# Optimization experiments

Hardware: AMD Instinct MI355X
Metric: run time of the kernel (lower is better)

Reference implementation:

```python
import jax, jax.numpy as jnp
import numpy as np

D = 192      # model dim (out_channels)
DIN = 384    # d_inner = 2*D
N = 16       # d_state
DTR = 12     # dt_rank = ceil(D/16)
K = 4        # depthwise conv kernel size
NB = 3       # total mamba blocks (2 stacked + 1 in downsample)


def setup_inputs() -> dict:
    key = jax.random.key(0)
    ks = jax.random.split(key, 8)
    rn = lambda k, shape, s: jax.random.normal(k, shape, jnp.float32) * s
    inp = {
        "x": jax.random.normal(ks[0], (2, 96, 56, 56), jnp.float32),
        "proj_w": rn(ks[1], (D, 96), 0.1),
        "proj_b": jnp.zeros((D,), jnp.float32),
        "bn_g": jnp.ones((D,), jnp.float32),
        "bn_b": jnp.zeros((D,), jnp.float32),
        "bn_mean": jnp.zeros((D,), jnp.float32),
        "bn_var": jnp.ones((D,), jnp.float32),
        "ln_g": jnp.ones((NB, D), jnp.float32),
        "ln_b": jnp.zeros((NB, D), jnp.float32),
        "Win": rn(ks[2], (NB, 2 * DIN, D), 0.05),
        "b_in": jnp.zeros((NB, 2 * DIN), jnp.float32),
        "conv_w": rn(ks[3], (NB, DIN, K), 0.2),
        "conv_b": jnp.zeros((NB, DIN), jnp.float32),
        "Wx": rn(ks[4], (NB, DTR + 2 * N, DIN), 0.05),
        "Wdt": rn(ks[5], (NB, DIN, DTR), 0.05),
        "bdt": jnp.full((NB, DIN), -4.6, jnp.float32),  # softplus ~ 0.01
        "A_log": jnp.log(jnp.broadcast_to(jnp.arange(1, N + 1, dtype=jnp.float32), (NB, DIN, N))),
        "Dskip": jnp.ones((NB, DIN), jnp.float32),
        "Wout": rn(ks[6], (NB, D, DIN), 0.05),
        "bout": jnp.zeros((NB, D), jnp.float32),
    }
    return inp


def _mamba(x, ln_g, ln_b, Win, b_in, conv_w, conv_b, Wx, Wdt, bdt, A_log, Dskip, Wout, bout):
    # x: (B, C, H, W) -> flatten spatial dims to a sequence (B, L, C)
    B, C, H, W = x.shape
    L = H * W
    seq = x.reshape(B, C, L).transpose(0, 2, 1)
    mu = seq.mean(-1, keepdims=True)
    var = seq.var(-1, keepdims=True)
    h = (seq - mu) * jax.lax.rsqrt(var + 1e-5) * ln_g + ln_b  # LayerNorm
    xz = jnp.einsum('bld,ed->ble', h, Win) + b_in              # (B, L, 2*DIN)
    xi, z = jnp.split(xz, 2, axis=-1)
    # depthwise causal conv1d along L
    xc = jnp.pad(xi.transpose(0, 2, 1), ((0, 0), (0, 0), (K - 1, 0)))
    xc = jax.lax.conv_general_dilated(xc, conv_w[:, None, :], (1,), 'VALID',
                                      feature_group_count=DIN) + conv_b[:, None]
    xi = jax.nn.silu(xc).transpose(0, 2, 1)                    # (B, L, DIN)
    proj = jnp.einsum('ble,pe->blp', xi, Wx)                   # (B, L, DTR+2N)
    dtl = proj[..., :DTR]
    Bm = proj[..., DTR:DTR + N]
    Cm = proj[..., DTR + N:]
    dt = jax.nn.softplus(jnp.einsum('blr,er->ble', dtl, Wdt) + bdt)  # (B, L, DIN)
    A = -jnp.exp(A_log)                                         # (DIN, N)
    dA = jnp.exp(dt[..., None] * A)                             # (B, L, DIN, N)
    dBx = (dt * xi)[..., None] * Bm[:, :, None, :]              # (B, L, DIN, N)

    def step(hc, t):
        dA_t, dBx_t, C_t = t
        hc = dA_t * hc + dBx_t                                  # (B, DIN, N)
        return hc, jnp.einsum('ben,bn->be', hc, C_t)

    h0 = jnp.zeros((B, DIN, N), x.dtype)
    _, ys = jax.lax.scan(step, h0, (dA.transpose(1, 0, 2, 3),
                                    dBx.transpose(1, 0, 2, 3),
                                    Cm.transpose(1, 0, 2)))
    y = ys.transpose(1, 0, 2) + Dskip * xi
    y = y * jax.nn.silu(z)
    out = jnp.einsum('ble,de->bld', y, Wout) + bout
    return out.transpose(0, 2, 1).reshape(B, C, H, W)


def _maxpool2(x):
    return jax.lax.reduce_window(x, -jnp.inf, jax.lax.max,
                                 (1, 1, 2, 2), (1, 1, 2, 2), 'VALID')


def reference(x, proj_w, proj_b, bn_g, bn_b, bn_mean, bn_var, ln_g, ln_b, Win, b_in,
              conv_w, conv_b, Wx, Wdt, bdt, A_log, Dskip, Wout, bout):
    # proj (conv1x1) + BatchNorm (eval-mode running stats)
    x = jnp.einsum('bchw,oc->bohw', x, proj_w) + proj_b[:, None, None]
    x = (x - bn_mean[:, None, None]) * jax.lax.rsqrt(bn_var[:, None, None] + 1e-5) \
        * bn_g[:, None, None] + bn_b[:, None, None]
    blk = lambda i, v: _mamba(v, ln_g[i], ln_b[i], Win[i], b_in[i], conv_w[i], conv_b[i],
                              Wx[i], Wdt[i], bdt[i], A_log[i], Dskip[i], Wout[i], bout[i])
    for i in range(2):  # residual mamba blocks
        x = x + blk(i, x)
    skip = x
    x = blk(2, _maxpool2(x))  # downsample: maxpool then mamba (no residual)
    return (x, skip)
```

## Files before the change

kernel.cpp:

```cpp
#include <hip/hip_runtime.h>

typedef __attribute__((ext_vector_type(8))) __bf16 bf16x8;
typedef __attribute__((ext_vector_type(4))) __bf16 bf16x4;
typedef __attribute__((ext_vector_type(4))) float f32x4;

#define DEV static __device__ __forceinline__

DEV float fast_rcp(float x) { return __builtin_amdgcn_rcpf(x); }
DEV float sigm(float x) { return fast_rcp(1.f + __expf(-x)); }
DEV float siluf(float x) { return x * sigm(x); }
DEV float softplusf(float x) { return x > 20.f ? x : __logf(1.f + __expf(x)); }

__global__ __launch_bounds__(256) void k_proj_wcvt(
    const float* __restrict__ x, const float* __restrict__ pw,
    const float* __restrict__ pb, const float* __restrict__ bng,
    const float* __restrict__ bnb, const float* __restrict__ bnm,
    const float* __restrict__ bnv, float* __restrict__ v,
    const float* __restrict__ Win, const float* __restrict__ Wout,
    const float* __restrict__ Wx, __bf16* __restrict__ Wb)
{
  constexpr int SAP = 104;
  __shared__ __bf16 As[64 * SAP];
  __shared__ __bf16 Ws[64 * SAP];
  const int tid = threadIdx.x;
  const int bid = blockIdx.x;

  if (bid >= 294) {
    const int idx = (bid - 294) * 256 + tid;
    if (idx < 442368) Wb[idx] = (__bf16)Win[idx];
    else if (idx < 663552) Wb[idx] = (__bf16)Wout[idx - 442368];
    else Wb[idx] = (__bf16)Wx[idx - 663552];
    return;
  }

  const int r0 = (bid % 98) * 64;
  const int col0 = (bid / 98) * 64;
  const int b = r0 / 3136, l0 = r0 % 3136;
  const int lane = tid & 63, wv = tid >> 6;
  const int rh = wv >> 1, ch = wv & 1;
  const int lm = lane & 15, quad = lane >> 4;

#pragma unroll
  for (int it = 0; it < 6; ++it) {
    const int idx = tid + it * 256;
    const int c = idx >> 4, l4 = idx & 15;
    const float4 t = *(const float4*)(x + ((size_t)(b * 96 + c)) * 3136 + l0 + l4 * 4);
    As[(l4 * 4 + 0) * SAP + c] = (__bf16)t.x;
    As[(l4 * 4 + 1) * SAP + c] = (__bf16)t.y;
    As[(l4 * 4 + 2) * SAP + c] = (__bf16)t.z;
    As[(l4 * 4 + 3) * SAP + c] = (__bf16)t.w;
  }
#pragma unroll
  for (int it = 0; it < 6; ++it) {
    const int idx = tid + it * 256;
    const int wr = idx / 24, kc = (idx % 24) * 4;
    const float4 t = *(const float4*)(pw + (size_t)(col0 + wr) * 96 + kc);
    bf16x4 o;
    o[0] = (__bf16)t.x; o[1] = (__bf16)t.y; o[2] = (__bf16)t.z; o[3] = (__bf16)t.w;
    *(bf16x4*)(&Ws[wr * SAP + kc]) = o;
  }
  __syncthreads();

  f32x4 acc[2][2] = {};
#pragma unroll
  for (int ks = 0; ks < 3; ++ks) {
    const int kb = ks * 32 + quad * 8;
    bf16x8 a0 = *(const bf16x8*)(&As[(rh * 32 + lm) * SAP + kb]);
    bf16x8 a1 = *(const bf16x8*)(&As[(rh * 32 + 16 + lm) * SAP + kb]);
    bf16x8 b0 = *(const bf16x8*)(&Ws[(ch * 32 + lm) * SAP + kb]);
    bf16x8 b1 = *(const bf16x8*)(&Ws[(ch * 32 + 16 + lm) * SAP + kb]);
    acc[0][0] = __builtin_amdgcn_mfma_f32_16x16x32_bf16(a0, b0, acc[0][0], 0, 0, 0);
    acc[0][1] = __builtin_amdgcn_mfma_f32_16x16x32_bf16(a0, b1, acc[0][1], 0, 0, 0);
    acc[1][0] = __builtin_amdgcn_mfma_f32_16x16x32_bf16(a1, b0, acc[1][0], 0, 0, 0);
    acc[1][1] = __builtin_amdgcn_mfma_f32_16x16x32_bf16(a1, b1, acc[1][1], 0, 0, 0);
  }

#pragma unroll
  for (int ti = 0; ti < 2; ++ti)
#pragma unroll
    for (int tj = 0; tj < 2; ++tj) {
      const int gcol = col0 + ch * 32 + tj * 16 + lm;
      const float s = rsqrtf(bnv[gcol] + 1e-5f) * bng[gcol];
      const float sh = (pb[gcol] - bnm[gcol]) * s + bnb[gcol];
#pragma unroll
      for (int j = 0; j < 4; ++j) {
        const int grow = r0 + rh * 32 + ti * 16 + quad * 4 + j;
        v[(size_t)grow * 192 + gcol] = acc[ti][tj][j] * s + sh;
      }
    }
}

__global__ __launch_bounds__(256) void k_conv(
    const float* __restrict__ xz, __bf16* __restrict__ xiB,
    const float* __restrict__ cw, const float* __restrict__ cb,
    int Lseq, int nthreads)
{
  const int idx = blockIdx.x * 256 + threadIdx.x;
  if (idx >= nthreads) return;
  const int e = idx % 384;
  const int seg = idx / 384;
  const int nseg = Lseq / 8;
  const int b = seg / nseg;
  const int l0 = (seg % nseg) * 8;
  const float4 w4 = *(const float4*)(cw + e * 4);
  const float bv = cb[e];
  float xv[11];
#pragma unroll
  for (int k = 0; k < 11; ++k) {
    const int l = l0 - 3 + k;
    xv[k] = (l >= 0) ? xz[(size_t)(b * Lseq + l) * 768 + e] : 0.f;
  }
#pragma unroll
  for (int j = 0; j < 8; ++j) {
    const float a = bv + xv[j] * w4.x + xv[j + 1] * w4.y + xv[j + 2] * w4.z + xv[j + 3] * w4.w;
    xiB[(size_t)(b * Lseq + l0 + j) * 384 + e] = (__bf16)siluf(a);
  }
}

constexpr int EPI_XZ = 0, EPI_G2 = 1, EPI_RES = 2, EPI_RES_SKIP = 3, EPI_OUT2 = 4;

template <int AMODE, int NT, int EPI>
__global__ __launch_bounds__(256) void k_gemm(
    const void* __restrict__ Ain, const __bf16* __restrict__ W,
    const float* __restrict__ bias, float* __restrict__ O,
    int M, int K, int Nvalid,
    float* __restrict__ dtlbuf, float* __restrict__ bcbuf,
    float* __restrict__ oflt,
    const float* __restrict__ lng, const float* __restrict__ lnb,
    int Lseq)
{
  constexpr int SA = 200;
  constexpr int CT = (NT == 1) ? 2 : 4;
  __shared__ __bf16 As[64 * SA];
  __shared__ __bf16 Ws[64 * NT * SA];
  __shared__ float lnS[(AMODE >= 2) ? 384 : 1];
  const int tid = threadIdx.x;
  const int r0 = blockIdx.x * 64;
  const int col0 = blockIdx.y * (64 * NT);
  const int lane = tid & 63, wv = tid >> 6;
  const int rh = (NT == 1) ? (wv >> 1) : (wv & 1);
  const int ch = (NT == 1) ? (wv & 1) : (wv >> 1);
  const int lm = lane & 15, quad = lane >> 4;

  if constexpr (AMODE >= 2) {
    if (tid < 192) { lnS[tid] = lng[tid]; lnS[192 + tid] = lnb[tid]; }
    __syncthreads();
  }

  f32x4 acc[2][CT] = {};
  const int nkp = K / 192;
  for (int kp = 0; kp < nkp; ++kp) {
    if (kp) __syncthreads();
    if constexpr (AMODE == 1) {
      const __bf16* Ab = (const __bf16*)Ain;
#pragma unroll
      for (int it = 0; it < 6; ++it) {
        const int idx = tid + it * 256;
        const int row = idx / 24, kc = (idx % 24) * 8;
        const int gr = min(r0 + row, M - 1);
        bf16x8 val = *(const bf16x8*)(Ab + (size_t)gr * K + kp * 192 + kc);
        *(bf16x8*)(&As[row * SA + kc]) = val;
      }
    } else {
      const float* A = (const float*)Ain;
      const int row = tid >> 2, part = tid & 3;
      const int gr = min(r0 + row, M - 1);
      const int cbase = part * 48;
      float4 tv[12];
      if constexpr (AMODE == 2) {
#pragma unroll
        for (int j = 0; j < 12; ++j)
          tv[j] = *(const float4*)(A + (size_t)gr * 192 + cbase + j * 4);
      } else {
        const int bb = gr / 784, l2 = gr % 784;
        const int h2 = l2 / 28, w2 = l2 % 28;
        const float* p0 = A + (size_t)(bb * 3136 + h2 * 112 + w2 * 2) * 192;
#pragma unroll
        for (int j = 0; j < 12; ++j) {
          const int cc = cbase + j * 4;
          const float4 a0 = *(const float4*)(p0 + cc);
          const float4 a1 = *(const float4*)(p0 + 192 + cc);
          const float4 a2 = *(const float4*)(p0 + 56 * 192 + cc);
          const float4 a3 = *(const float4*)(p0 + 57 * 192 + cc);
          tv[j].x = fmaxf(fmaxf(a0.x, a1.x), fmaxf(a2.x, a3.x));
          tv[j].y = fmaxf(fmaxf(a0.y, a1.y), fmaxf(a2.y, a3.y));
          tv[j].z = fmaxf(fmaxf(a0.z, a1.z), fmaxf(a2.z, a3.z));
          tv[j].w = fmaxf(fmaxf(a0.w, a1.w), fmaxf(a2.w, a3.w));
        }
      }
      float s = 0.f, sq = 0.f;
#pragma unroll
      for (int j = 0; j < 12; ++j) {
        s += tv[j].x + tv[j].y + tv[j].z + tv[j].w;
        sq += tv[j].x * tv[j].x + tv[j].y * tv[j].y + tv[j].z * tv[j].z + tv[j].w * tv[j].w;
      }
      s += __shfl_xor(s, 1); s += __shfl_xor(s, 2);
      sq += __shfl_xor(sq, 1); sq += __shfl_xor(sq, 2);
      const float mean = s * (1.f / 192.f);
      const float rstd = rsqrtf(sq * (1.f / 192.f) - mean * mean + 1e-5f);
#pragma unroll
      for (int j = 0; j < 12; ++j) {
        const int c = cbase + j * 4;
        bf16x4 o;
        o[0] = (__bf16)((tv[j].x - mean) * rstd * lnS[c + 0] + lnS[192 + c + 0]);
        o[1] = (__bf16)((tv[j].y - mean) * rstd * lnS[c + 1] + lnS[192 + c + 1]);
        o[2] = (__bf16)((tv[j].z - mean) * rstd * lnS[c + 2] + lnS[192 + c + 2]);
        o[3] = (__bf16)((tv[j].w - mean) * rstd * lnS[c + 3] + lnS[192 + c + 3]);
        *(bf16x4*)(&As[row * SA + c]) = o;
      }
    }
#pragma unroll
    for (int it = 0; it < 6 * NT; ++it) {
      const int idx = tid + it * 256;
      const int wr = idx / 24, kc = (idx % 24) * 8;
      const int gw = col0 + wr;
      bf16x8 val = {};
      if (gw < Nvalid) val = *(const bf16x8*)(W + (size_t)gw * K + kp * 192 + kc);
      *(bf16x8*)(&Ws[wr * SA + kc]) = val;
    }
    __syncthreads();
#pragma unroll
    for (int ks = 0; ks < 6; ++ks) {
      const int kb = ks * 32 + quad * 8;
      bf16x8 a0 = *(const bf16x8*)(&As[(rh * 32 + lm) * SA + kb]);
      bf16x8 a1 = *(const bf16x8*)(&As[(rh * 32 + 16 + lm) * SA + kb]);
#pragma unroll
      for (int tj = 0; tj < CT; ++tj) {
        bf16x8 bfr = *(const bf16x8*)(&Ws[(ch * (16 * CT) + tj * 16 + lm) * SA + kb]);
        acc[0][tj] = __builtin_amdgcn_mfma_f32_16x16x32_bf16(a0, bfr, acc[0][tj], 0, 0, 0);
        acc[1][tj] = __builtin_amdgcn_mfma_f32_16x16x32_bf16(a1, bfr, acc[1][tj], 0, 0, 0);
      }
    }
  }

  if constexpr (EPI == EPI_G2) {
    __shared__ float dtlS[64 * 12];
#pragma unroll
    for (int ti = 0; ti < 2; ++ti)
#pragma unroll
      for (int tj = 0; tj < CT; ++tj) {
        const int colt = ch * (16 * CT) + tj * 16 + lm;
#pragma unroll
        for (int j = 0; j < 4; ++j) {
          const int rowt = rh * 32 + ti * 16 + quad * 4 + j;
          const int grow = r0 + rowt;
          const float val = acc[ti][tj][j];
          if (colt < 12) dtlS[rowt * 12 + colt] = val;
          else if (colt < 44 && grow < M)
            bcbuf[(size_t)grow * 32 + (colt - 12)] = val;
        }
      }
    __syncthreads();
    for (int idx = tid; idx < 64 * 12; idx += 256) {
      const int grow = r0 + idx / 12;
      if (grow < M) dtlbuf[(size_t)grow * 12 + idx % 12] = dtlS[idx];
    }
  } else {
#pragma unroll
    for (int ti = 0; ti < 2; ++ti)
#pragma unroll
      for (int tj = 0; tj < CT; ++tj) {
        const int colt = ch * (16 * CT) + tj * 16 + lm;
        const int gcol = col0 + colt;
        const float bv = bias[gcol];
#pragma unroll
        for (int j = 0; j < 4; ++j) {
          const int rowt = rh * 32 + ti * 16 + quad * 4 + j;
          const int grow = r0 + rowt;
          if (grow >= M) continue;
          const float val = acc[ti][tj][j] + bv;
          if constexpr (EPI == EPI_XZ) {
            O[(size_t)grow * 768 + gcol] = val;
          } else if constexpr (EPI == EPI_RES) {
            O[(size_t)grow * 192 + gcol] += val;
          } else if constexpr (EPI == EPI_RES_SKIP) {
            const float nv = O[(size_t)grow * 192 + gcol] + val;
            O[(size_t)grow * 192 + gcol] = nv;
            const int b = grow / 3136, l = grow % 3136;
            oflt[b * 602112 + gcol * 3136 + l] = nv;
          } else {
            const int b = grow / 784, l = grow % 784;
            oflt[b * 150528 + gcol * 784 + l] = val;
          }
        }
      }
  }
}

constexpr int SC_LC = 14, SC_T = 7, SC_TN = 2;

DEV void compute_dts(const float* __restrict__ dtl, const float* __restrict__ Wdt,
                     const float* __restrict__ bdt, int rowbase, int e, int t,
                     float* dtlS, float* wdtS)
{
  for (int idx = t; idx < SC_LC * 12; idx += 128)
    dtlS[idx] = dtl[(size_t)(rowbase + idx / 12) * 12 + idx % 12];
#pragma unroll
  for (int r = 0; r < 12; ++r) wdtS[r * 128 + t] = Wdt[(size_t)e * 12 + r];
}

__global__ __launch_bounds__(128) void k_scan1(
    const float* __restrict__ dtl, const __bf16* __restrict__ xi,
    const float* __restrict__ bc, const float* __restrict__ Wdt,
    const float* __restrict__ bdt, const float* __restrict__ A_log,
    float* __restrict__ DT, float* __restrict__ S, int Lseq, int NC)
{
  __shared__ float Bs[SC_LC * 16];
  __shared__ float dts[SC_LC * 128];
  __shared__ float dtlS[SC_LC * 12];
  __shared__ float wdtS[12 * 128];
  const int t = threadIdx.x;
  const int e = blockIdx.y * 128 + t;
  const int c = blockIdx.x % NC;
  const int b = blockIdx.x / NC;
  const int rowbase = b * Lseq + c * SC_LC;

  for (int idx = t; idx < SC_LC * 16; idx += 128) {
    const int l = idx >> 4, q = idx & 15;
    Bs[idx] = bc[(size_t)(rowbase + l) * 32 + q];
  }
  compute_dts(dtl, Wdt, bdt, rowbase, e, t, dtlS, wdtS);
  const float bdte = bdt[e];

  float An2[16];
  {
    const float4* a4 = (const float4*)(A_log + e * 16);
    float4 t0 = a4[0], t1 = a4[1], t2 = a4[2], t3 = a4[3];
    float tmp[16] = {t0.x, t0.y, t0.z, t0.w, t1.x, t1.y, t1.z, t1.w,
                     t2.x, t2.y, t2.z, t2.w, t3.x, t3.y, t3.z, t3.w};
#pragma unroll
    for (int n = 0; n < 16; ++n) An2[n] = -__expf(tmp[n]) * 1.44269504f;
  }
  __syncthreads();
  float dtsum = 0.f;
  for (int l = 0; l < SC_LC; ++l) {
    float a = bdte;
#pragma unroll
    for (int r = 0; r < 12; ++r) a += dtlS[l * 12 + r] * wdtS[r * 128 + t];
    const float sp = softplusf(a);
    dts[l * 128 + t] = sp;
    dtsum += sp;
  }

  float h[16];
#pragma unroll
  for (int n = 0; n < 16; ++n) h[n] = 0.f;

  float xA[SC_T], xB[SC_T];
  auto LOADA = [&](int tt) {
#pragma unroll
    for (int j = 0; j < SC_T; ++j)
      xA[j] = (float)xi[(size_t)(rowbase + tt * SC_T + j) * 384 + e];
  };
  auto LOADB = [&](int tt) {
#pragma unroll
    for (int j = 0; j < SC_T; ++j)
      xB[j] = (float)xi[(size_t)(rowbase + tt * SC_T + j) * 384 + e];
  };
  auto COMP = [&](const float (&x8)[SC_T], int tt) {
#pragma unroll
    for (int j = 0; j < SC_T; ++j) {
      const int l = tt * SC_T + j;
      const float dtv = dts[l * 128 + t];
      const float u = dtv * x8[j];
      const float* Brow = &Bs[l * 16];
#pragma unroll
      for (int n = 0; n < 16; ++n) {
        const float a = __builtin_amdgcn_exp2f(dtv * An2[n]);
        h[n] = a * h[n] + u * Brow[n];
      }
    }
  };

  LOADA(0);
#pragma unroll
  for (int tt = 0; tt < SC_TN; ++tt) {
    if (tt & 1) { if (tt + 1 < SC_TN) LOADA(tt + 1); COMP(xB, tt); }
    else        { if (tt + 1 < SC_TN) LOADB(tt + 1); COMP(xA, tt); }
  }

  const size_t o = ((size_t)(b * NC + c) * 384 + e) * 16;
#pragma unroll
  for (int q = 0; q < 4; ++q)
    *(float4*)(S + o + q * 4) = make_float4(h[q*4], h[q*4+1], h[q*4+2], h[q*4+3]);
  DT[(size_t)(b * NC + c) * 384 + e] = dtsum;
}

__global__ __launch_bounds__(256) void k_carry(
    const float* __restrict__ DT, float* __restrict__ SH,
    const float* __restrict__ A_log, int NC)
{
  const int tid = blockIdx.x * 256 + threadIdx.x;
  const int b = tid / 6144, r = tid % 6144;
  const float An2 = -__expf(A_log[r]) * 1.44269504f;
  const size_t o = (size_t)b * NC * 6144 + r;
  const size_t od = (size_t)b * NC * 384 + (r >> 4);

  float sA[8], dA[8], sB[8], dB[8];
  auto LOAD = [&](float (&sv)[8], float (&dv)[8], int c0) {
#pragma unroll
    for (int k = 0; k < 8; ++k) {
      sv[k] = SH[o + (size_t)(c0 + k) * 6144];
      dv[k] = DT[od + (size_t)(c0 + k) * 384];
    }
  };
  float h = 0.f;
  auto COMP = [&](const float (&sv)[8], const float (&dv)[8], int c0) {
    float a[8];
#pragma unroll
    for (int k = 0; k < 8; ++k) a[k] = __builtin_amdgcn_exp2f(An2 * dv[k]);
#pragma unroll
    for (int k = 0; k < 8; ++k) {
      SH[o + (size_t)(c0 + k) * 6144] = h;
      h = a[k] * h + sv[k];
    }
  };

  LOAD(sA, dA, 0);
  for (int c0 = 0; c0 < NC; c0 += 16) {
    if (c0 + 8 < NC) LOAD(sB, dB, c0 + 8);
    COMP(sA, dA, c0);
    if (c0 + 8 < NC) {
      if (c0 + 16 < NC) LOAD(sA, dA, c0 + 16);
      COMP(sB, dB, c0 + 8);
    }
  }
}

__global__ __launch_bounds__(128) void k_scan2(
    const float* __restrict__ dtl, const __bf16* __restrict__ xi,
    const float* __restrict__ bc, const float* __restrict__ xz,
    const float* __restrict__ Wdt, const float* __restrict__ bdt,
    const float* __restrict__ A_log, const float* __restrict__ Dskip,
    const float* __restrict__ H0, __bf16* __restrict__ y, int Lseq, int NC)
{
  __shared__ float BCs[SC_LC * 32];
  __shared__ float dts[SC_LC * 128];
  __shared__ float dtlS[SC_LC * 12];
  __shared__ float wdtS[12 * 128];
  const int t = threadIdx.x;
  const int e = blockIdx.y * 128 + t;
  const int c = blockIdx.x % NC;
  const int b = blockIdx.x / NC;
  const int rowbase = b * Lseq + c * SC_LC;

  for (int idx = t; idx < SC_LC * 32; idx += 128)
    BCs[idx] = bc[(size_t)rowbase * 32 + idx];
  compute_dts(dtl, Wdt, bdt, rowbase, e, t, dtlS, wdtS);
  const float bdte = bdt[e];

  float An2[16];
  {
    const float4* a4 = (const float4*)(A_log + e * 16);
    float4 t0 = a4[0], t1 = a4[1], t2 = a4[2], t3 = a4[3];
    float tmp[16] = {t0.x, t0.y, t0.z, t0.w, t1.x, t1.y, t1.z, t1.w,
                     t2.x, t2.y, t2.z, t2.w, t3.x, t3.y, t3.z, t3.w};
#pragma unroll
    for (int n = 0; n < 16; ++n) An2[n] = -__expf(tmp[n]) * 1.44269504f;
  }
  float h[16];
  {
    const size_t o = ((size_t)(b * NC + c) * 384 + e) * 16;
    const float4* h4 = (const float4*)(H0 + o);
    float4 t0 = h4[0], t1 = h4[1], t2 = h4[2], t3 = h4[3];
    h[0]=t0.x; h[1]=t0.y; h[2]=t0.z; h[3]=t0.w;
    h[4]=t1.x; h[5]=t1.y; h[6]=t1.z; h[7]=t1.w;
    h[8]=t2.x; h[9]=t2.y; h[10]=t2.z; h[11]=t2.w;
    h[12]=t3.x; h[13]=t3.y; h[14]=t3.z; h[15]=t3.w;
  }
  __syncthreads();
  for (int l = 0; l < SC_LC; ++l) {
    float a = bdte;
#pragma unroll
    for (int r = 0; r < 12; ++r) a += dtlS[l * 12 + r] * wdtS[r * 128 + t];
    dts[l * 128 + t] = softplusf(a);
  }
  const float Dse = Dskip[e];

  float xA[SC_T], zA[SC_T], xB[SC_T], zB[SC_T];
  auto LOADA = [&](int tt) {
#pragma unroll
    for (int j = 0; j < SC_T; ++j) {
      const size_t r = (size_t)(rowbase + tt * SC_T + j);
      xA[j] = (float)xi[r * 384 + e];
      zA[j] = xz[r * 768 + 384 + e];
    }
  };
  auto LOADB = [&](int tt) {
#pragma unroll
    for (int j = 0; j < SC_T; ++j) {
      const size_t r = (size_t)(rowbase + tt * SC_T + j);
      xB[j] = (float)xi[r * 384 + e];
      zB[j] = xz[r * 768 + 384 + e];
    }
  };
  auto COMP = [&](const float (&x8)[SC_T], const float (&z8)[SC_T], int tt) {
#pragma unroll
    for (int j = 0; j < SC_T; ++j) {
      const int l = tt * SC_T + j;
      const float dtv = dts[l * 128 + t];
      const float xiv = x8[j];
      const float u = dtv * xiv;
      const float* Brow = &BCs[l * 32];
      const float* Crow = Brow + 16;
      float yv = 0.f;
#pragma unroll
      for (int n = 0; n < 16; ++n) {
        const float a = __builtin_amdgcn_exp2f(dtv * An2[n]);
        h[n] = a * h[n] + u * Brow[n];
        yv += h[n] * Crow[n];
      }
      y[(size_t)(rowbase + l) * 384 + e] = (__bf16)((yv + Dse * xiv) * siluf(z8[j]));
    }
  };

  LOADA(0);
#pragma unroll
  for (int tt = 0; tt < SC_TN; ++tt) {
    if (tt & 1) { if (tt + 1 < SC_TN) LOADA(tt + 1); COMP(xB, zB, tt); }
    else        { if (tt + 1 < SC_TN) LOADB(tt + 1); COMP(xA, zA, tt); }
  }
}

extern "C" void kernel_launch(void* const* d_in, const int* in_sizes, int n_in,
                              void* d_out, int out_size, void* d_ws, size_t ws_size,
                              hipStream_t stream)
{
  const float* x    = (const float*)d_in[0];
  const float* pw   = (const float*)d_in[1];
  const float* pb   = (const float*)d_in[2];
  const float* bng  = (const float*)d_in[3];
  const float* bnb  = (const float*)d_in[4];
  const float* bnm  = (const float*)d_in[5];
  const float* bnv  = (const float*)d_in[6];
  const float* lng  = (const float*)d_in[7];
  const float* lnb  = (const float*)d_in[8];
  const float* Win  = (const float*)d_in[9];
  const float* b_in = (const float*)d_in[10];
  const float* cw   = (const float*)d_in[11];
  const float* cb   = (const float*)d_in[12];
  const float* Wx   = (const float*)d_in[13];
  const float* Wdt  = (const float*)d_in[14];
  const float* bdt  = (const float*)d_in[15];
  const float* Alog = (const float*)d_in[16];
  const float* Dsk  = (const float*)d_in[17];
  const float* Wout = (const float*)d_in[18];
  const float* bout = (const float*)d_in[19];

  float* wsf = (float*)d_ws;
  float* v    = wsf;
  float* xz   = v + 1204224;
  float* dtlb = xz + 4816896;
  float* bcb  = dtlb + 75264;
  float* Sb   = bcb + 200704;
  float* Pb   = Sb + 2752512;
  __bf16* xiB = (__bf16*)(Pb + 2752512);
  __bf16* yB  = (__bf16*)(Pb + 2752512 + 1204224);
  __bf16* Wb  = (__bf16*)(Pb + 2752512 + 2408448);

  float* out0 = (float*)d_out;
  float* out1 = out0 + 301056;

  k_proj_wcvt<<<3084, 256, 0, stream>>>(x, pw, pb, bng, bnb, bnm, bnv, v,
                                        Win, Wout, Wx, Wb);

  for (int i = 0; i < 3; ++i) {
    const int big = (i < 2) ? 1 : 0;
    const int Lseq = big ? 3136 : 784;
    const int M = 2 * Lseq;
    const int NC = Lseq / SC_LC;
    const int MB = (M + 63) / 64;
    const float* lng_i = lng + i * 192;
    const float* lnb_i = lnb + i * 192;
    const float* bin_i = b_in + i * 768;
    const float* cw_i  = cw + i * 384 * 4;
    const float* cb_i  = cb + i * 384;
    const float* Wdt_i = Wdt + i * 384 * 12;
    const float* bdt_i = bdt + i * 384;
    const float* Al_i  = Alog + i * 384 * 16;
    const float* Ds_i  = Dsk + i * 384;
    const float* bo_i  = bout + i * 192;
    const __bf16* Winb_i  = Wb + i * 147456;
    const __bf16* Woutb_i = Wb + 442368 + i * 73728;
    const __bf16* Wxb_i   = Wb + 663552 + i * 16896;

    if (big)
      k_gemm<2, 2, EPI_XZ><<<dim3(MB, 6), 256, 0, stream>>>(
          v, Winb_i, bin_i, xz, M, 192, 768,
          nullptr, nullptr, nullptr, lng_i, lnb_i, Lseq);
    else
      k_gemm<3, 2, EPI_XZ><<<dim3(MB, 6), 256, 0, stream>>>(
          v, Winb_i, bin_i, xz, M, 192, 768,
          nullptr, nullptr, nullptr, lng_i, lnb_i, Lseq);
    k_conv<<<(M * 384 / 8 + 255) / 256, 256, 0, stream>>>(
        xz, xiB, cw_i, cb_i, Lseq, M * 384 / 8);
    k_gemm<1, 1, EPI_G2><<<dim3(MB, 1), 256, 0, stream>>>(
        xiB, Wxb_i, nullptr, nullptr, M, 384, 44,
        dtlb, bcb, nullptr, nullptr, nullptr, Lseq);
    k_scan1<<<dim3(2 * NC, 3), 128, 0, stream>>>(
        dtlb, xiB, bcb, Wdt_i, bdt_i, Al_i, Pb, Sb, Lseq, NC);
    k_carry<<<48, 256, 0, stream>>>(Pb, Sb, Al_i, NC);
    k_scan2<<<dim3(2 * NC, 3), 128, 0, stream>>>(
        dtlb, xiB, bcb, xz, Wdt_i, bdt_i, Al_i, Ds_i, Sb, yB, Lseq, NC);
    if (i == 0)
      k_gemm<1, 1, EPI_RES><<<dim3(MB, 3), 256, 0, stream>>>(
          yB, Woutb_i, bo_i, v, M, 384, 192,
          nullptr, nullptr, nullptr, nullptr, nullptr, Lseq);
    else if (i == 1)
      k_gemm<1, 1, EPI_RES_SKIP><<<dim3(MB, 3), 256, 0, stream>>>(
          yB, Woutb_i, bo_i, v, M, 384, 192,
          nullptr, nullptr, out1, nullptr, nullptr, Lseq);
    else
      k_gemm<1, 1, EPI_OUT2><<<dim3(MB, 3), 256, 0, stream>>>(
          yB, Woutb_i, bo_i, v, M, 384, 192,
          nullptr, nullptr, out0, nullptr, nullptr, Lseq);
  }
}
```

Before: 358.4 us.

## Fuse depthwise causal conv and SiLU into in-projection GEMM epilogue

```diff
diff --git a/kernel.cpp b/kernel.cpp
--- a/kernel.cpp
+++ b/kernel.cpp
@@ -10,6 +10,7 @@
 DEV float sigm(float x) { return fast_rcp(1.f + __expf(-x)); }
 DEV float siluf(float x) { return x * sigm(x); }
 DEV float softplusf(float x) { return x > 20.f ? x : __logf(1.f + __expf(x)); }
+
 
 __global__ __launch_bounds__(256) void k_proj_wcvt(
     const float* __restrict__ x, const float* __restrict__ pw,
@@ -26,10 +27,18 @@
   const int bid = blockIdx.x;
 
   if (bid >= 294) {
-    const int idx = (bid - 294) * 256 + tid;
-    if (idx < 442368) Wb[idx] = (__bf16)Win[idx];
-    else if (idx < 663552) Wb[idx] = (__bf16)Wout[idx - 442368];
-    else Wb[idx] = (__bf16)Wx[idx - 663552];
+    const int idx = ((bid - 294) * 256 + tid) * 4;
+    if (idx < 714240) {
+      const float* src;
+      if (idx < 442368) src = Win + idx;
+      else if (idx < 663552) src = Wout + (idx - 442368);
+      else src = Wx + (idx - 663552);
+      const float4 tv = *(const float4*)src;
+      bf16x4 o;
+      o[0] = (__bf16)tv.x; o[1] = (__bf16)tv.y;
+      o[2] = (__bf16)tv.z; o[3] = (__bf16)tv.w;
+      *(bf16x4*)(Wb + idx) = o;
+    }
     return;
   }
 
@@ -90,33 +99,6 @@
     }
 }
 
-__global__ __launch_bounds__(256) void k_conv(
-    const float* __restrict__ xz, __bf16* __restrict__ xiB,
-    const float* __restrict__ cw, const float* __restrict__ cb,
-    int Lseq, int nthreads)
-{
-  const int idx = blockIdx.x * 256 + threadIdx.x;
-  if (idx >= nthreads) return;
-  const int e = idx % 384;
-  const int seg = idx / 384;
-  const int nseg = Lseq / 8;
-  const int b = seg / nseg;
-  const int l0 = (seg % nseg) * 8;
-  const float4 w4 = *(const float4*)(cw + e * 4);
-  const float bv = cb[e];
-  float xv[11];
-#pragma unroll
-  for (int k = 0; k < 11; ++k) {
-    const int l = l0 - 3 + k;
-    xv[k] = (l >= 0) ? xz[(size_t)(b * Lseq + l) * 768 + e] : 0.f;
-  }
-#pragma unroll
-  for (int j = 0; j < 8; ++j) {
-    const float a = bv + xv[j] * w4.x + xv[j + 1] * w4.y + xv[j + 2] * w4.z + xv[j + 3] * w4.w;
-    xiB[(size_t)(b * Lseq + l0 + j) * 384 + e] = (__bf16)siluf(a);
-  }
-}
-
 constexpr int EPI_XZ = 0, EPI_G2 = 1, EPI_RES = 2, EPI_RES_SKIP = 3, EPI_OUT2 = 4;
 
 template <int AMODE, int NT, int EPI>
@@ -127,13 +109,22 @@
     float* __restrict__ dtlbuf, float* __restrict__ bcbuf,
     float* __restrict__ oflt,
     const float* __restrict__ lng, const float* __restrict__ lnb,
-    int Lseq)
+    int Lseq, const float* __restrict__ cw, const float* __restrict__ cbv)
 {
   constexpr int SA = 200;
   constexpr int CT = (NT == 1) ? 2 : 4;
-  __shared__ __bf16 As[64 * SA];
-  __shared__ __bf16 Ws[64 * NT * SA];
-  __shared__ float lnS[(AMODE >= 2) ? 384 : 1];
+  constexpr int A_ROWS = (AMODE >= 2) ? 67 : 64;
+  constexpr int ABYTES = A_ROWS * SA * 2;
+  constexpr int WBYTES = 64 * NT * SA * 2;
+  constexpr int LBYTES = (AMODE >= 2) ? 384 * 4 : 0;
+  constexpr int XBYTES = (EPI == EPI_XZ) ? 67 * 132 * 4 : (EPI == EPI_G2 ? 64 * 12 * 4 : 0);
+  constexpr int MAINB = ABYTES + WBYTES + LBYTES;
+  constexpr int SMEMB = MAINB > XBYTES ? MAINB : XBYTES;
+  __shared__ __align__(16) char smem[SMEMB];
+  __bf16* As = (__bf16*)smem;
+  __bf16* Ws = (__bf16*)(smem + ABYTES);
+  float* lnS = (float*)(smem + ABYTES + WBYTES);
+
   const int tid = threadIdx.x;
   const int r0 = blockIdx.x * 64;
   const int col0 = blockIdx.y * (64 * NT);
@@ -163,50 +154,60 @@
       }
     } else {
       const float* A = (const float*)Ain;
-      const int row = tid >> 2, part = tid & 3;
-      const int gr = min(r0 + row, M - 1);
+      const int part = tid & 3;
       const int cbase = part * 48;
-      float4 tv[12];
-      if constexpr (AMODE == 2) {
-#pragma unroll
-        for (int j = 0; j < 12; ++j)
-          tv[j] = *(const float4*)(A + (size_t)gr * 192 + cbase + j * 4);
-      } else {
-        const int bb = gr / 784, l2 = gr % 784;
-        const int h2 = l2 / 28, w2 = l2 % 28;
-        const float* p0 = A + (size_t)(bb * 3136 + h2 * 112 + w2 * 2) * 192;
+      auto STAGE_ROW = [&](int row_slot, int gr) {
+        float4 tv[12];
+        if constexpr (AMODE == 2) {
+#pragma unroll
+          for (int j = 0; j < 12; ++j)
+            tv[j] = *(const float4*)(A + (size_t)gr * 192 + cbase + j * 4);
+        } else {
+          const int bb = gr / 784, l2 = gr % 784;
+          const int h2 = l2 / 28, w2 = l2 % 28;
+          const float* p0 = A + (size_t)(bb * 3136 + h2 * 112 + w2 * 2) * 192;
+#pragma unroll
+          for (int j = 0; j < 12; ++j) {
+            const int cc2 = cbase + j * 4;
+            const float4 a0 = *(const float4*)(p0 + cc2);
+            const float4 a1 = *(const float4*)(p0 + 192 + cc2);
+            const float4 a2 = *(const float4*)(p0 + 56 * 192 + cc2);
+            const float4 a3 = *(const float4*)(p0 + 57 * 192 + cc2);
+            tv[j].x = fmaxf(fmaxf(a0.x, a1.x), fmaxf(a2.x, a3.x));
+            tv[j].y = fmaxf(fmaxf(a0.y, a1.y), fmaxf(a2.y, a3.y));
+            tv[j].z = fmaxf(fmaxf(a0.z, a1.z), fmaxf(a2.z, a3.z));
+            tv[j].w = fmaxf(fmaxf(a0.w, a1.w), fmaxf(a2.w, a3.w));
+          }
+        }
+        float s = 0.f, sq = 0.f;
 #pragma unroll
         for (int j = 0; j < 12; ++j) {
-          const int cc = cbase + j * 4;
-          const float4 a0 = *(const float4*)(p0 + cc);
-          const float4 a1 = *(const float4*)(p0 + 192 + cc);
-          const float4 a2 = *(const float4*)(p0 + 56 * 192 + cc);
-          const float4 a3 = *(const float4*)(p0 + 57 * 192 + cc);
-          tv[j].x = fmaxf(fmaxf(a0.x, a1.x), fmaxf(a2.x, a3.x));
-          tv[j].y = fmaxf(fmaxf(a0.y, a1.y), fmaxf(a2.y, a3.y));
-          tv[j].z = fmaxf(fmaxf(a0.z, a1.z), fmaxf(a2.z, a3.z));
-          tv[j].w = fmaxf(fmaxf(a0.w, a1.w), fmaxf(a2.w, a3.w));
-        }
-      }
-      float s = 0.f, sq = 0.f;
-#pragma unroll
-      for (int j = 0; j < 12; ++j) {
-        s += tv[j].x + tv[j].y + tv[j].z + tv[j].w;
-        sq += tv[j].x * tv[j].x + tv[j].y * tv[j].y + tv[j].z * tv[j].z + tv[j].w * tv[j].w;
-      }
-      s += __shfl_xor(s, 1); s += __shfl_xor(s, 2);
-      sq += __shfl_xor(sq, 1); sq += __shfl_xor(sq, 2);
-      const float mean = s * (1.f / 192.f);
-      const float rstd = rsqrtf(sq * (1.f / 192.f) - mean * mean + 1e-5f);
-#pragma unroll
-      for (int j = 0; j < 12; ++j) {
-        const int c = cbase + j * 4;
-        bf16x4 o;
-        o[0] = (__bf16)((tv[j].x - mean) * rstd * lnS[c + 0] + lnS[192 + c + 0]);
-        o[1] = (__bf16)((tv[j].y - mean) * rstd * lnS[c + 1] + lnS[192 + c + 1]);
-        o[2] = (__bf16)((tv[j].z - mean) * rstd * lnS[c + 2] + lnS[192 + c + 2]);
-        o[3] = (__bf16)((tv[j].w - mean) * rstd * lnS[c + 3] + lnS[192 + c + 3]);
-        *(bf16x4*)(&As[row * SA + c]) = o;
+          s += tv[j].x + tv[j].y + tv[j].z + tv[j].w;
+          sq += tv[j].x * tv[j].x + tv[j].y * tv[j].y + tv[j].z * tv[j].z + tv[j].w * tv[j].w;
+        }
+        s += __shfl_xor(s, 1); s += __shfl_xor(s, 2);
+        sq += __shfl_xor(sq, 1); sq += __shfl_xor(sq, 2);
+        const float mean = s * (1.f / 192.f);
+        const float rstd = rsqrtf(sq * (1.f / 192.f) - mean * mean + 1e-5f);
+#pragma unroll
+        for (int j = 0; j < 12; ++j) {
+          const int c = cbase + j * 4;
+          bf16x4 o;
+          o[0] = (__bf16)((tv[j].x - mean) * rstd * lnS[c + 0] + lnS[192 + c + 0]);
+          o[1] = (__bf16)((tv[j].y - mean) * rstd * lnS[c + 1] + lnS[192 + c + 1]);
+          o[2] = (__bf16)((tv[j].z - mean) * rstd * lnS[c + 2] + lnS[192 + c + 2]);
+          o[3] = (__bf16)((tv[j].w - mean) * rstd * lnS[c + 3] + lnS[192 + c + 3]);
+          *(bf16x4*)(&As[row_slot * SA + c]) = o;
+        }
+      };
+      STAGE_ROW(tid >> 2, min(r0 + (tid >> 2), M - 1));
+      if constexpr (EPI == EPI_XZ) {
+        if (tid < 12) {
+          const int hrow = tid >> 2;
+          int gh = r0 - 3 + hrow;
+          gh = gh < 0 ? 0 : gh;
+          STAGE_ROW(64 + hrow, gh);
+        }
       }
     }
 #pragma unroll
@@ -234,7 +235,8 @@
   }
 
   if constexpr (EPI == EPI_G2) {
-    __shared__ float dtlS[64 * 12];
+    __syncthreads();
+    float* dtlS = (float*)smem;
 #pragma unroll
     for (int ti = 0; ti < 2; ++ti)
 #pragma unroll
@@ -255,6 +257,80 @@
       const int grow = r0 + idx / 12;
       if (grow < M) dtlbuf[(size_t)grow * 12 + idx % 12] = dtlS[idx];
     }
+  } else if constexpr (EPI == EPI_XZ) {
+    if (AMODE >= 2 && col0 < 384) {
+      auto HDOT = [&](int hr, int hc) -> float {
+        const __bf16* ap = &As[(64 + hr) * SA];
+        const __bf16* wp = &Ws[hc * SA];
+        float d = 0.f;
+#pragma unroll
+        for (int k8 = 0; k8 < 24; ++k8) {
+          bf16x8 av = *(const bf16x8*)(ap + k8 * 8);
+          bf16x8 wv8 = *(const bf16x8*)(wp + k8 * 8);
+#pragma unroll
+          for (int u = 0; u < 8; ++u) d += (float)av[u] * (float)wv8[u];
+        }
+        return d + bias[col0 + hc];
+      };
+      const int hr0 = tid >> 7, hc0 = tid & 127;
+      const bool has1 = tid < 128;
+      const float hv0 = HDOT(hr0, hc0);
+      float hv1 = 0.f;
+      if (has1) hv1 = HDOT(2, hc0);
+      __syncthreads();
+      float* xcS = (float*)smem;
+#pragma unroll
+      for (int ti = 0; ti < 2; ++ti)
+#pragma unroll
+        for (int tj = 0; tj < CT; ++tj) {
+          const int colt = ch * (16 * CT) + tj * 16 + lm;
+          const float bv = bias[col0 + colt];
+#pragma unroll
+          for (int j = 0; j < 4; ++j) {
+            const int rowt = rh * 32 + ti * 16 + quad * 4 + j;
+            xcS[(rowt + 3) * 132 + colt] = acc[ti][tj][j] + bv;
+          }
+        }
+      xcS[hr0 * 132 + hc0] = hv0;
+      if (has1) xcS[2 * 132 + hc0] = hv1;
+      __syncthreads();
+      const int cc = tid & 127;
+      const int rbase = tid >> 7;
+      const int gcol = col0 + cc;
+      const float4 w4 = *(const float4*)(cw + gcol * 4);
+      const float cbe = cbv[gcol];
+      __bf16* xout = (__bf16*)oflt;
+#pragma unroll
+      for (int k2 = 0; k2 < 32; ++k2) {
+        const int lt = rbase + k2 * 2;
+        const int grow = r0 + lt;
+        if (grow >= M) break;
+        const int l = grow < Lseq ? grow : grow - Lseq;
+        const float* xp = &xcS[lt * 132 + cc];
+        float a = cbe;
+        a += (l >= 3 ? xp[0]   : 0.f) * w4.x;
+        a += (l >= 2 ? xp[132] : 0.f) * w4.y;
+        a += (l >= 1 ? xp[264] : 0.f) * w4.z;
+        a += xp[396] * w4.w;
+        xout[(size_t)grow * 384 + gcol] = (__bf16)siluf(a);
+      }
+    } else {
+#pragma unroll
+      for (int ti = 0; ti < 2; ++ti)
+#pragma unroll
+        for (int tj = 0; tj < CT; ++tj) {
+          const int colt = ch * (16 * CT) + tj * 16 + lm;
+          const int gcol = col0 + colt;
+          const float bv = bias[gcol];
+#pragma unroll
+          for (int j = 0; j < 4; ++j) {
+            const int rowt = rh * 32 + ti * 16 + quad * 4 + j;
+            const int grow = r0 + rowt;
+            if (grow >= M) continue;
+            O[(size_t)grow * 768 + gcol] = acc[ti][tj][j] + bv;
+          }
+        }
+    }
   } else {
 #pragma unroll
     for (int ti = 0; ti < 2; ++ti)
@@ -269,9 +345,7 @@
           const int grow = r0 + rowt;
           if (grow >= M) continue;
           const float val = acc[ti][tj][j] + bv;
-          if constexpr (EPI == EPI_XZ) {
-            O[(size_t)grow * 768 + gcol] = val;
-          } else if constexpr (EPI == EPI_RES) {
+          if constexpr (EPI == EPI_RES) {
             O[(size_t)grow * 192 + gcol] += val;
           } else if constexpr (EPI == EPI_RES_SKIP) {
             const float nv = O[(size_t)grow * 192 + gcol] + val;
@@ -561,8 +635,8 @@
   float* out0 = (float*)d_out;
   float* out1 = out0 + 301056;
 
-  k_proj_wcvt<<<3084, 256, 0, stream>>>(x, pw, pb, bng, bnb, bnm, bnv, v,
-                                        Win, Wout, Wx, Wb);
+  k_proj_wcvt<<<992, 256, 0, stream>>>(x, pw, pb, bng, bnb, bnm, bnv, v,
+                                       Win, Wout, Wx, Wb);
 
   for (int i = 0; i < 3; ++i) {
     const int big = (i < 2) ? 1 : 0;
@@ -587,16 +661,14 @@
     if (big)
       k_gemm<2, 2, EPI_XZ><<<dim3(MB, 6), 256, 0, stream>>>(
           v, Winb_i, bin_i, xz, M, 192, 768,
-          nullptr, nullptr, nullptr, lng_i, lnb_i, Lseq);
+          nullptr, nullptr, (float*)xiB, lng_i, lnb_i, Lseq, cw_i, cb_i);
     else
       k_gemm<3, 2, EPI_XZ><<<dim3(MB, 6), 256, 0, stream>>>(
           v, Winb_i, bin_i, xz, M, 192, 768,
-          nullptr, nullptr, nullptr, lng_i, lnb_i, Lseq);
-    k_conv<<<(M * 384 / 8 + 255) / 256, 256, 0, stream>>>(
-        xz, xiB, cw_i, cb_i, Lseq, M * 384 / 8);
+          nullptr, nullptr, (float*)xiB, lng_i, lnb_i, Lseq, cw_i, cb_i);
     k_gemm<1, 1, EPI_G2><<<dim3(MB, 1), 256, 0, stream>>>(
         xiB, Wxb_i, nullptr, nullptr, M, 384, 44,
-        dtlb, bcb, nullptr, nullptr, nullptr, Lseq);
+        dtlb, bcb, nullptr, nullptr, nullptr, Lseq, nullptr, nullptr);
     k_scan1<<<dim3(2 * NC, 3), 128, 0, stream>>>(
         dtlb, xiB, bcb, Wdt_i, bdt_i, Al_i, Pb, Sb, Lseq, NC);
     k_carry<<<48, 256, 0, stream>>>(Pb, Sb, Al_i, NC);
@@ -605,14 +677,14 @@
     if (i == 0)
       k_gemm<1, 1, EPI_RES><<<dim3(MB, 3), 256, 0, stream>>>(
           yB, Woutb_i, bo_i, v, M, 384, 192,
-          nullptr, nullptr, nullptr, nullptr, nullptr, Lseq);
+          nullptr, nullptr, nullptr, nullptr, nullptr, Lseq, nullptr, nullptr);
     else if (i == 1)
       k_gemm<1, 1, EPI_RES_SKIP><<<dim3(MB, 3), 256, 0, stream>>>(
           yB, Woutb_i, bo_i, v, M, 384, 192,
-          nullptr, nullptr, out1, nullptr, nullptr, Lseq);
+          nullptr, nullptr, out1, nullptr, nullptr, Lseq, nullptr, nullptr);
     else
       k_gemm<1, 1, EPI_OUT2><<<dim3(MB, 3), 256, 0, stream>>>(
           yB, Woutb_i, bo_i, v, M, 384, 192,
-          nullptr, nullptr, out0, nullptr, nullptr, Lseq);
+          nullptr, nullptr, out0, nullptr, nullptr, Lseq, nullptr, nullptr);
   }
 }
```

New measurement: 392.8 us. 9.6% more time.

## Split xz GEMM into dedicated kernel reading weights directly, vectorize weight conversion

Applied to the files above, without the earlier changes.

```diff
diff --git a/kernel.cpp b/kernel.cpp
--- a/kernel.cpp
+++ b/kernel.cpp
@@ -10,6 +10,7 @@
 DEV float sigm(float x) { return fast_rcp(1.f + __expf(-x)); }
 DEV float siluf(float x) { return x * sigm(x); }
 DEV float softplusf(float x) { return x > 20.f ? x : __logf(1.f + __expf(x)); }
+
 
 __global__ __launch_bounds__(256) void k_proj_wcvt(
     const float* __restrict__ x, const float* __restrict__ pw,
@@ -26,10 +27,18 @@
   const int bid = blockIdx.x;
 
   if (bid >= 294) {
-    const int idx = (bid - 294) * 256 + tid;
-    if (idx < 442368) Wb[idx] = (__bf16)Win[idx];
-    else if (idx < 663552) Wb[idx] = (__bf16)Wout[idx - 442368];
-    else Wb[idx] = (__bf16)Wx[idx - 663552];
+    const int idx = ((bid - 294) * 256 + tid) * 4;
+    if (idx < 714240) {
+      const float* src;
+      if (idx < 442368) src = Win + idx;
+      else if (idx < 663552) src = Wout + (idx - 442368);
+      else src = Wx + (idx - 663552);
+      const float4 tv = *(const float4*)src;
+      bf16x4 o;
+      o[0] = (__bf16)tv.x; o[1] = (__bf16)tv.y;
+      o[2] = (__bf16)tv.z; o[3] = (__bf16)tv.w;
+      *(bf16x4*)(Wb + idx) = o;
+    }
     return;
   }
 
@@ -117,100 +126,138 @@
   }
 }
 
-constexpr int EPI_XZ = 0, EPI_G2 = 1, EPI_RES = 2, EPI_RES_SKIP = 3, EPI_OUT2 = 4;
-
-template <int AMODE, int NT, int EPI>
+template <int AMODE>
+__global__ __launch_bounds__(256, 4) void k_gemm_xz(
+    const float* __restrict__ A, const __bf16* __restrict__ W,
+    const float* __restrict__ bias, float* __restrict__ O,
+    int M, const float* __restrict__ lng, const float* __restrict__ lnb)
+{
+  constexpr int SA = 200;
+  __shared__ __bf16 As[64 * SA];
+  __shared__ float lnS[384];
+  const int tid = threadIdx.x;
+  const int r0 = blockIdx.x * 64;
+  const int col0 = blockIdx.y * 128;
+  const int lane = tid & 63, wv = tid >> 6;
+  const int rh = wv & 1, ch = wv >> 1;
+  const int lm = lane & 15, quad = lane >> 4;
+
+  if (tid < 192) { lnS[tid] = lng[tid]; lnS[192 + tid] = lnb[tid]; }
+  __syncthreads();
+
+  {
+    const int row = tid >> 2, part = tid & 3;
+    const int gr = min(r0 + row, M - 1);
+    const int cbase = part * 48;
+    float4 tv[12];
+    if constexpr (AMODE == 2) {
+#pragma unroll
+      for (int j = 0; j < 12; ++j)
+        tv[j] = *(const float4*)(A + (size_t)gr * 192 + cbase + j * 4);
+    } else {
+      const int bb = gr / 784, l2 = gr % 784;
+      const int h2 = l2 / 28, w2 = l2 % 28;
+      const float* p0 = A + (size_t)(bb * 3136 + h2 * 112 + w2 * 2) * 192;
+#pragma unroll
+      for (int j = 0; j < 12; ++j) {
+        const int cc = cbase + j * 4;
+        const float4 a0 = *(const float4*)(p0 + cc);
+        const float4 a1 = *(const float4*)(p0 + 192 + cc);
+        const float4 a2 = *(const float4*)(p0 + 56 * 192 + cc);
+        const float4 a3 = *(const float4*)(p0 + 57 * 192 + cc);
+        tv[j].x = fmaxf(fmaxf(a0.x, a1.x), fmaxf(a2.x, a3.x));
+        tv[j].y = fmaxf(fmaxf(a0.y, a1.y), fmaxf(a2.y, a3.y));
+        tv[j].z = fmaxf(fmaxf(a0.z, a1.z), fmaxf(a2.z, a3.z));
+        tv[j].w = fmaxf(fmaxf(a0.w, a1.w), fmaxf(a2.w, a3.w));
+      }
+    }
+    float s = 0.f, sq = 0.f;
+#pragma unroll
+    for (int j = 0; j < 12; ++j) {
+      s += tv[j].x + tv[j].y + tv[j].z + tv[j].w;
+      sq += tv[j].x * tv[j].x + tv[j].y * tv[j].y + tv[j].z * tv[j].z + tv[j].w * tv[j].w;
+    }
+    s += __shfl_xor(s, 1); s += __shfl_xor(s, 2);
+    sq += __shfl_xor(sq, 1); sq += __shfl_xor(sq, 2);
+    const float mean = s * (1.f / 192.f);
+    const float rstd = rsqrtf(sq * (1.f / 192.f) - mean * mean + 1e-5f);
+#pragma unroll
+    for (int j = 0; j < 12; ++j) {
+      const int c = cbase + j * 4;
+      bf16x4 o;
+      o[0] = (__bf16)((tv[j].x - mean) * rstd * lnS[c + 0] + lnS[192 + c + 0]);
+      o[1] = (__bf16)((tv[j].y - mean) * rstd * lnS[c + 1] + lnS[192 + c + 1]);
+      o[2] = (__bf16)((tv[j].z - mean) * rstd * lnS[c + 2] + lnS[192 + c + 2]);
+      o[3] = (__bf16)((tv[j].w - mean) * rstd * lnS[c + 3] + lnS[192 + c + 3]);
+      *(bf16x4*)(&As[row * SA + c]) = o;
+    }
+  }
+  __syncthreads();
+
+  f32x4 acc[2][4] = {};
+#pragma unroll
+  for (int ks = 0; ks < 6; ++ks) {
+    const int kb = ks * 32 + quad * 8;
+    bf16x8 a0 = *(const bf16x8*)(&As[(rh * 32 + lm) * SA + kb]);
+    bf16x8 a1 = *(const bf16x8*)(&As[(rh * 32 + 16 + lm) * SA + kb]);
+#pragma unroll
+    for (int tj = 0; tj < 4; ++tj) {
+      const int gw = col0 + ch * 64 + tj * 16 + lm;
+      bf16x8 bfr = *(const bf16x8*)(W + (size_t)gw * 192 + kb);
+      acc[0][tj] = __builtin_amdgcn_mfma_f32_16x16x32_bf16(a0, bfr, acc[0][tj], 0, 0, 0);
+      acc[1][tj] = __builtin_amdgcn_mfma_f32_16x16x32_bf16(a1, bfr, acc[1][tj], 0, 0, 0);
+    }
+  }
+
+#pragma unroll
+  for (int ti = 0; ti < 2; ++ti)
+#pragma unroll
+    for (int tj = 0; tj < 4; ++tj) {
+      const int gcol = col0 + ch * 64 + tj * 16 + lm;
+      const float bv = bias[gcol];
+#pragma unroll
+      for (int j = 0; j < 4; ++j) {
+        const int rowt = rh * 32 + ti * 16 + quad * 4 + j;
+        const int grow = r0 + rowt;
+        if (grow < M) O[(size_t)grow * 768 + gcol] = acc[ti][tj][j] + bv;
+      }
+    }
+}
+
+constexpr int EPI_G2 = 1, EPI_RES = 2, EPI_RES_SKIP = 3, EPI_OUT2 = 4;
+
+template <int EPI>
 __global__ __launch_bounds__(256) void k_gemm(
-    const void* __restrict__ Ain, const __bf16* __restrict__ W,
+    const __bf16* __restrict__ Ab, const __bf16* __restrict__ W,
     const float* __restrict__ bias, float* __restrict__ O,
     int M, int K, int Nvalid,
     float* __restrict__ dtlbuf, float* __restrict__ bcbuf,
-    float* __restrict__ oflt,
-    const float* __restrict__ lng, const float* __restrict__ lnb,
-    int Lseq)
+    float* __restrict__ oflt)
 {
   constexpr int SA = 200;
-  constexpr int CT = (NT == 1) ? 2 : 4;
   __shared__ __bf16 As[64 * SA];
-  __shared__ __bf16 Ws[64 * NT * SA];
-  __shared__ float lnS[(AMODE >= 2) ? 384 : 1];
+  __shared__ __bf16 Ws[64 * SA];
   const int tid = threadIdx.x;
   const int r0 = blockIdx.x * 64;
-  const int col0 = blockIdx.y * (64 * NT);
+  const int col0 = blockIdx.y * 64;
   const int lane = tid & 63, wv = tid >> 6;
-  const int rh = (NT == 1) ? (wv >> 1) : (wv & 1);
-  const int ch = (NT == 1) ? (wv & 1) : (wv >> 1);
+  const int rh = wv >> 1, ch = wv & 1;
   const int lm = lane & 15, quad = lane >> 4;
 
-  if constexpr (AMODE >= 2) {
-    if (tid < 192) { lnS[tid] = lng[tid]; lnS[192 + tid] = lnb[tid]; }
-    __syncthreads();
-  }
-
-  f32x4 acc[2][CT] = {};
+  f32x4 acc[2][2] = {};
   const int nkp = K / 192;
   for (int kp = 0; kp < nkp; ++kp) {
     if (kp) __syncthreads();
-    if constexpr (AMODE == 1) {
-      const __bf16* Ab = (const __bf16*)Ain;
-#pragma unroll
-      for (int it = 0; it < 6; ++it) {
-        const int idx = tid + it * 256;
-        const int row = idx / 24, kc = (idx % 24) * 8;
-        const int gr = min(r0 + row, M - 1);
-        bf16x8 val = *(const bf16x8*)(Ab + (size_t)gr * K + kp * 192 + kc);
-        *(bf16x8*)(&As[row * SA + kc]) = val;
-      }
-    } else {
-      const float* A = (const float*)Ain;
-      const int row = tid >> 2, part = tid & 3;
+#pragma unroll
+    for (int it = 0; it < 6; ++it) {
+      const int idx = tid + it * 256;
+      const int row = idx / 24, kc = (idx % 24) * 8;
       const int gr = min(r0 + row, M - 1);
-      const int cbase = part * 48;
-      float4 tv[12];
-      if constexpr (AMODE == 2) {
-#pragma unroll
-        for (int j = 0; j < 12; ++j)
-          tv[j] = *(const float4*)(A + (size_t)gr * 192 + cbase + j * 4);
-      } else {
-        const int bb = gr / 784, l2 = gr % 784;
-        const int h2 = l2 / 28, w2 = l2 % 28;
-        const float* p0 = A + (size_t)(bb * 3136 + h2 * 112 + w2 * 2) * 192;
-#pragma unroll
-        for (int j = 0; j < 12; ++j) {
-          const int cc = cbase + j * 4;
-          const float4 a0 = *(const float4*)(p0 + cc);
-          const float4 a1 = *(const float4*)(p0 + 192 + cc);
-          const float4 a2 = *(const float4*)(p0 + 56 * 192 + cc);
-          const float4 a3 = *(const float4*)(p0 + 57 * 192 + cc);
-          tv[j].x = fmaxf(fmaxf(a0.x, a1.x), fmaxf(a2.x, a3.x));
-          tv[j].y = fmaxf(fmaxf(a0.y, a1.y), fmaxf(a2.y, a3.y));
-          tv[j].z = fmaxf(fmaxf(a0.z, a1.z), fmaxf(a2.z, a3.z));
-          tv[j].w = fmaxf(fmaxf(a0.w, a1.w), fmaxf(a2.w, a3.w));
-        }
-      }
-      float s = 0.f, sq = 0.f;
-#pragma unroll
-      for (int j = 0; j < 12; ++j) {
-        s += tv[j].x + tv[j].y + tv[j].z + tv[j].w;
-        sq += tv[j].x * tv[j].x + tv[j].y * tv[j].y + tv[j].z * tv[j].z + tv[j].w * tv[j].w;
-      }
-      s += __shfl_xor(s, 1); s += __shfl_xor(s, 2);
-      sq += __shfl_xor(sq, 1); sq += __shfl_xor(sq, 2);
-      const float mean = s * (1.f / 192.f);
-      const float rstd = rsqrtf(sq * (1.f / 192.f) - mean * mean + 1e-5f);
-#pragma unroll
-      for (int j = 0; j < 12; ++j) {
-        const int c = cbase + j * 4;
-        bf16x4 o;
-        o[0] = (__bf16)((tv[j].x - mean) * rstd * lnS[c + 0] + lnS[192 + c + 0]);
-        o[1] = (__bf16)((tv[j].y - mean) * rstd * lnS[c + 1] + lnS[192 + c + 1]);
-        o[2] = (__bf16)((tv[j].z - mean) * rstd * lnS[c + 2] + lnS[192 + c + 2]);
-        o[3] = (__bf16)((tv[j].w - mean) * rstd * lnS[c + 3] + lnS[192 + c + 3]);
-        *(bf16x4*)(&As[row * SA + c]) = o;
-      }
-    }
-#pragma unroll
-    for (int it = 0; it < 6 * NT; ++it) {
+      bf16x8 val = *(const bf16x8*)(Ab + (size_t)gr * K + kp * 192 + kc);
+      *(bf16x8*)(&As[row * SA + kc]) = val;
+    }
+#pragma unroll
+    for (int it = 0; it < 6; ++it) {
       const int idx = tid + it * 256;
       const int wr = idx / 24, kc = (idx % 24) * 8;
       const int gw = col0 + wr;
@@ -225,8 +272,8 @@
       bf16x8 a0 = *(const bf16x8*)(&As[(rh * 32 + lm) * SA + kb]);
       bf16x8 a1 = *(const bf16x8*)(&As[(rh * 32 + 16 + lm) * SA + kb]);
 #pragma unroll
-      for (int tj = 0; tj < CT; ++tj) {
-        bf16x8 bfr = *(const bf16x8*)(&Ws[(ch * (16 * CT) + tj * 16 + lm) * SA + kb]);
+      for (int tj = 0; tj < 2; ++tj) {
+        bf16x8 bfr = *(const bf16x8*)(&Ws[(ch * 32 + tj * 16 + lm) * SA + kb]);
         acc[0][tj] = __builtin_amdgcn_mfma_f32_16x16x32_bf16(a0, bfr, acc[0][tj], 0, 0, 0);
         acc[1][tj] = __builtin_amdgcn_mfma_f32_16x16x32_bf16(a1, bfr, acc[1][tj], 0, 0, 0);
       }
@@ -238,8 +285,8 @@
 #pragma unroll
     for (int ti = 0; ti < 2; ++ti)
 #pragma unroll
-      for (int tj = 0; tj < CT; ++tj) {
-        const int colt = ch * (16 * CT) + tj * 16 + lm;
+      for (int tj = 0; tj < 2; ++tj) {
+        const int colt = ch * 32 + tj * 16 + lm;
 #pragma unroll
         for (int j = 0; j < 4; ++j) {
           const int rowt = rh * 32 + ti * 16 + quad * 4 + j;
@@ -259,8 +306,8 @@
 #pragma unroll
     for (int ti = 0; ti < 2; ++ti)
 #pragma unroll
-      for (int tj = 0; tj < CT; ++tj) {
-        const int colt = ch * (16 * CT) + tj * 16 + lm;
+      for (int tj = 0; tj < 2; ++tj) {
+        const int colt = ch * 32 + tj * 16 + lm;
         const int gcol = col0 + colt;
         const float bv = bias[gcol];
 #pragma unroll
@@ -269,9 +316,7 @@
           const int grow = r0 + rowt;
           if (grow >= M) continue;
           const float val = acc[ti][tj][j] + bv;
-          if constexpr (EPI == EPI_XZ) {
-            O[(size_t)grow * 768 + gcol] = val;
-          } else if constexpr (EPI == EPI_RES) {
+          if constexpr (EPI == EPI_RES) {
             O[(size_t)grow * 192 + gcol] += val;
           } else if constexpr (EPI == EPI_RES_SKIP) {
             const float nv = O[(size_t)grow * 192 + gcol] + val;
@@ -561,8 +606,8 @@
   float* out0 = (float*)d_out;
   float* out1 = out0 + 301056;
 
-  k_proj_wcvt<<<3084, 256, 0, stream>>>(x, pw, pb, bng, bnb, bnm, bnv, v,
-                                        Win, Wout, Wx, Wb);
+  k_proj_wcvt<<<992, 256, 0, stream>>>(x, pw, pb, bng, bnb, bnm, bnv, v,
+                                       Win, Wout, Wx, Wb);
 
   for (int i = 0; i < 3; ++i) {
     const int big = (i < 2) ? 1 : 0;
@@ -585,34 +630,28 @@
     const __bf16* Wxb_i   = Wb + 663552 + i * 16896;
 
     if (big)
-      k_gemm<2, 2, EPI_XZ><<<dim3(MB, 6), 256, 0, stream>>>(
-          v, Winb_i, bin_i, xz, M, 192, 768,
-          nullptr, nullptr, nullptr, lng_i, lnb_i, Lseq);
+      k_gemm_xz<2><<<dim3(MB, 6), 256, 0, stream>>>(
+          v, Winb_i, bin_i, xz, M, lng_i, lnb_i);
     else
-      k_gemm<3, 2, EPI_XZ><<<dim3(MB, 6), 256, 0, stream>>>(
-          v, Winb_i, bin_i, xz, M, 192, 768,
-          nullptr, nullptr, nullptr, lng_i, lnb_i, Lseq);
+      k_gemm_xz<3><<<dim3(MB, 6), 256, 0, stream>>>(
+          v, Winb_i, bin_i, xz, M, lng_i, lnb_i);
     k_conv<<<(M * 384 / 8 + 255) / 256, 256, 0, stream>>>(
         xz, xiB, cw_i, cb_i, Lseq, M * 384 / 8);
-    k_gemm<1, 1, EPI_G2><<<dim3(MB, 1), 256, 0, stream>>>(
-        xiB, Wxb_i, nullptr, nullptr, M, 384, 44,
-        dtlb, bcb, nullptr, nullptr, nullptr, Lseq);
+    k_gemm<EPI_G2><<<dim3(MB, 1), 256, 0, stream>>>(
+        xiB, Wxb_i, nullptr, nullptr, M, 384, 44, dtlb, bcb, nullptr);
     k_scan1<<<dim3(2 * NC, 3), 128, 0, stream>>>(
         dtlb, xiB, bcb, Wdt_i, bdt_i, Al_i, Pb, Sb, Lseq, NC);
     k_carry<<<48, 256, 0, stream>>>(Pb, Sb, Al_i, NC);
     k_scan2<<<dim3(2 * NC, 3), 128, 0, stream>>>(
         dtlb, xiB, bcb, xz, Wdt_i, bdt_i, Al_i, Ds_i, Sb, yB, Lseq, NC);
     if (i == 0)
-      k_gemm<1, 1, EPI_RES><<<dim3(MB, 3), 256, 0, stream>>>(
-          yB, Woutb_i, bo_i, v, M, 384, 192,
-          nullptr, nullptr, nullptr, nullptr, nullptr, Lseq);
+      k_gemm<EPI_RES><<<dim3(MB, 3), 256, 0, stream>>>(
+          yB, Woutb_i, bo_i, v, M, 384, 192, nullptr, nullptr, nullptr);
     else if (i == 1)
-      k_gemm<1, 1, EPI_RES_SKIP><<<dim3(MB, 3), 256, 0, stream>>>(
-          yB, Woutb_i, bo_i, v, M, 384, 192,
-          nullptr, nullptr, out1, nullptr, nullptr, Lseq);
+      k_gemm<EPI_RES_SKIP><<<dim3(MB, 3), 256, 0, stream>>>(
+          yB, Woutb_i, bo_i, v, M, 384, 192, nullptr, nullptr, out1);
     else
-      k_gemm<1, 1, EPI_OUT2><<<dim3(MB, 3), 256, 0, stream>>>(
-          yB, Woutb_i, bo_i, v, M, 384, 192,
-          nullptr, nullptr, out0, nullptr, nullptr, Lseq);
-  }
-}
+      k_gemm<EPI_OUT2><<<dim3(MB, 3), 256, 0, stream>>>(
+          yB, Woutb_i, bo_i, v, M, 384, 192, nullptr, nullptr, out0);
+  }
+}
```

Measured after the change: 354.6 us. About the same (-1.1%).
